# Kernel optimization log

Measured on AMD Instinct MI355X. Metric: run time of the kernel, lower is better.

## Reference

```python
import jax, jax.numpy as jnp
import numpy as np

NUM_EXPERTS = 8
HIDDEN = 1024
TOKENS = 8192


def setup_inputs() -> dict:
    key = jax.random.key(0)
    k1, k2, k3, k4 = jax.random.split(key, 4)
    inp = jax.random.normal(k1, (TOKENS, HIDDEN), dtype=jnp.float32)
    gate = jax.random.normal(k2, (TOKENS, NUM_EXPERTS), dtype=jnp.float32)
    # expert parameters: one dense layer per expert (H -> H)
    W = jax.random.normal(k3, (NUM_EXPERTS, HIDDEN, HIDDEN), dtype=jnp.float32) / np.sqrt(HIDDEN)
    b = jax.random.normal(k4, (NUM_EXPERTS, HIDDEN), dtype=jnp.float32) * 0.01
    return {"input": inp, "gate": gate, "W": W, "b": b}


def reference(input, gate, W, b):
    # Routing: softmax over router logits, top-1 expert per token.
    probs = jax.nn.softmax(gate, axis=-1)            # [T, E]
    expert_idx = jnp.argmax(probs, axis=-1)          # [T]
    top_p = jnp.take_along_axis(probs, expert_idx[:, None], axis=-1)[:, 0]  # [T]

    # Dispatch + grouped GEMM (computed densely for all experts, then masked):
    # y[e, t, d] = input[t, :] @ W[e] + b[e]
    y = jnp.einsum("th,ehd->etd", input, W) + b[:, None, :]  # [E, T, H]

    # Combine: select the routed expert's output, scaled by its gate prob.
    dispatch = jax.nn.one_hot(expert_idx, NUM_EXPERTS, dtype=input.dtype) * top_p[:, None]  # [T, E]
    out = jnp.einsum("etd,te->td", y, dispatch)      # [T, H]
    return out
```

## Files before the change

### kernel.cpp

```cpp
#include <hip/hip_runtime.h>
#include <hip/hip_bf16.h>
#include <cstdint>
#include <cstddef>

#define TOK 8192
#define HID 1024
#define NE 8

typedef __bf16 bf16x4 __attribute__((ext_vector_type(4)));
typedef __bf16 bf16x8 __attribute__((ext_vector_type(8)));
typedef float floatx4 __attribute__((ext_vector_type(4)));

static __device__ __forceinline__ __bf16 f2bf(float x) {
    unsigned u = __builtin_bit_cast(unsigned, x);
    u += 0x7fffu + ((u >> 16) & 1u);
    unsigned short hs = (unsigned short)(u >> 16);
    return __builtin_bit_cast(__bf16, hs);
}

__global__ void prep_kernel(const float* __restrict__ X, const float* __restrict__ gate,
                            const float* __restrict__ W,
                            __bf16* __restrict__ Xb, __bf16* __restrict__ Wt,
                            float* __restrict__ scale, int* __restrict__ counts,
                            int* __restrict__ list) {
    const int b = blockIdx.x;
    const int t = threadIdx.x;

    if (b < 4096) {
        size_t idx = (size_t)b * 256 + t;
        const float4 a0 = *(const float4*)(X + idx * 8);
        const float4 a1 = *(const float4*)(X + idx * 8 + 4);
        bf16x8 v;
        v[0] = f2bf(a0.x); v[1] = f2bf(a0.y); v[2] = f2bf(a0.z); v[3] = f2bf(a0.w);
        v[4] = f2bf(a1.x); v[5] = f2bf(a1.y); v[6] = f2bf(a1.z); v[7] = f2bf(a1.w);
        *(bf16x8*)(Xb + idx * 8) = v;

        if (b < 32) {
            __shared__ int hcnt[NE];
            __shared__ int hbase[NE];
            if (t < NE) hcnt[t] = 0;
            __syncthreads();
            int tok = b * 256 + t;
            float g[NE];
#pragma unroll
            for (int j = 0; j < NE; j++) g[j] = gate[tok * NE + j];
            float gm = g[0]; int best = 0;
#pragma unroll
            for (int j = 1; j < NE; j++) {
                if (g[j] > gm) { gm = g[j]; best = j; }
            }
            float s = 0.f;
#pragma unroll
            for (int j = 0; j < NE; j++) s += __expf(g[j] - gm);
            scale[tok] = 1.0f / s;
            int lpos = atomicAdd(&hcnt[best], 1);
            __syncthreads();
            if (t < NE) hbase[t] = atomicAdd(&counts[t], hcnt[t]);
            __syncthreads();
            list[best * TOK + hbase[best] + lpos] = tok;
        }
    } else {
        const int bb = b - 4096;
        const int e  = bb >> 6;
        const int kt = (bb >> 4) & 3;
        const int nt = bb & 15;
        const int k0 = kt * 256, n0 = nt * 64;
        const int ka = t >> 3;
        const int nb = t & 7;

        const float* src = W + ((size_t)e * HID + k0 + ka * 8) * HID + n0 + nb * 8;
        float rr[8][8];
#pragma unroll
        for (int i = 0; i < 8; i++) {
            float4 x = *(const float4*)(src + (size_t)i * HID);
            float4 y = *(const float4*)(src + (size_t)i * HID + 4);
            rr[i][0] = x.x; rr[i][1] = x.y; rr[i][2] = x.z; rr[i][3] = x.w;
            rr[i][4] = y.x; rr[i][5] = y.y; rr[i][6] = y.z; rr[i][7] = y.w;
        }
        __bf16* dst = Wt + ((size_t)e * HID + n0 + nb * 8) * HID + k0 + ka * 8;
#pragma unroll
        for (int j = 0; j < 8; j++) {
            bf16x8 v;
#pragma unroll
            for (int i = 0; i < 8; i++) v[i] = f2bf(rr[i][j]);
            *(bf16x8*)(dst + (size_t)j * HID) = v;
        }
    }
}

__launch_bounds__(256)
__global__ void moe_gemm_bf16(const __bf16* __restrict__ Xb, const __bf16* __restrict__ Wt,
                              const float* __restrict__ Bias, const float* __restrict__ scale,
                              const int* __restrict__ counts, const int* __restrict__ list,
                              float* __restrict__ out) {
    const int bid = blockIdx.x;
    const int e  = bid & 7;
    const int nt = (bid >> 3) & 15;
    const int mt = bid >> 7;

    const int cnt = counts[e];
    if (mt * 128 >= cnt) return;
    const int mvalid = min(128, cnt - mt * 128);
    const int n0 = nt * 64;

    __shared__ __bf16 As[128 * 64];
    __shared__ __bf16 Bs[64 * 64];
    __shared__ int   tok[128];
    __shared__ float scl[128];

    const int tid  = threadIdx.x;
    const int lane = tid & 63;
    const int wave = tid >> 6;

    if (tid < 128) {
        int g = mt * 128 + tid;
        int tk = (g < cnt) ? list[e * TOK + g] : 0;
        tok[tid] = tk;
        scl[tid] = (g < cnt) ? scale[tk] : 0.f;
    }
    __syncthreads();

    const int srow = lane >> 3;
    const int gchunk = ((lane & 7) ^ srow) * 8;
    const __bf16* aptr[4];
    const __bf16* bptr[2];
#pragma unroll
    for (int i = 0; i < 4; i++) {
        int r = wave * 32 + i * 8 + srow;
        aptr[i] = Xb + (size_t)tok[r] * HID + gchunk;
    }
#pragma unroll
    for (int i = 0; i < 2; i++) {
        int r = wave * 16 + i * 8 + srow;
        bptr[i] = Wt + ((size_t)e * HID + n0 + r) * HID + gchunk;
    }

    const int ln = lane & 15;
    const int q  = lane >> 4;
    const int wm = (wave >> 1) * 64;
    const int wn = (wave & 1) * 32;
    const int rsw = ln & 7;

    floatx4 acc[4][2];
#pragma unroll
    for (int mi = 0; mi < 4; mi++)
#pragma unroll
        for (int ni = 0; ni < 2; ni++) acc[mi][ni] = (floatx4){0.f, 0.f, 0.f, 0.f};

    for (int k0 = 0; k0 < HID; k0 += 64) {
#pragma unroll
        for (int i = 0; i < 4; i++)
            __builtin_amdgcn_global_load_lds(
                (const __attribute__((address_space(1))) void*)(aptr[i] + k0),
                (__attribute__((address_space(3))) void*)(&As[(wave * 32 + i * 8) * 64]),
                16, 0, 0);
#pragma unroll
        for (int i = 0; i < 2; i++)
            __builtin_amdgcn_global_load_lds(
                (const __attribute__((address_space(1))) void*)(bptr[i] + k0),
                (__attribute__((address_space(3))) void*)(&Bs[(wave * 16 + i * 8) * 64]),
                16, 0, 0);
        __syncthreads();

#pragma unroll
        for (int kk = 0; kk < 64; kk += 32) {
            const int cb = (kk >> 3) + q;
            const int pos = (cb ^ rsw) * 8;
            bf16x8 af[4], bfv[2];
#pragma unroll
            for (int mi = 0; mi < 4; mi++)
                af[mi] = *(const bf16x8*)(&As[(wm + mi * 16 + ln) * 64 + pos]);
#pragma unroll
            for (int ni = 0; ni < 2; ni++)
                bfv[ni] = *(const bf16x8*)(&Bs[(wn + ni * 16 + ln) * 64 + pos]);
#pragma unroll
            for (int mi = 0; mi < 4; mi++)
#pragma unroll
                for (int ni = 0; ni < 2; ni++)
                    acc[mi][ni] = __builtin_amdgcn_mfma_f32_16x16x32_bf16(
                        af[mi], bfv[ni], acc[mi][ni], 0, 0, 0);
        }
        __syncthreads();
    }

    float bn[2];
#pragma unroll
    for (int ni = 0; ni < 2; ni++) bn[ni] = Bias[e * HID + n0 + wn + ni * 16 + ln];

#pragma unroll
    for (int mi = 0; mi < 4; mi++) {
#pragma unroll
        for (int r = 0; r < 4; r++) {
            int row = wm + mi * 16 + q * 4 + r;
            if (row < mvalid) {
                int t = tok[row];
                float sc = scl[row];
                size_t ob = (size_t)t * HID + n0 + wn + ln;
#pragma unroll
                for (int ni = 0; ni < 2; ni++)
                    __builtin_nontemporal_store(sc * (acc[mi][ni][r] + bn[ni]),
                                                &out[ob + ni * 16]);
            }
        }
    }
}

__launch_bounds__(256)
__global__ void moe_gemm_fb(const float* __restrict__ X, const float* __restrict__ W,
                            const float* __restrict__ Bias, const float* __restrict__ scale,
                            const int* __restrict__ counts, const int* __restrict__ list,
                            float* __restrict__ out) {
    const int bid = blockIdx.x;
    const int e  = bid >> 9;
    const int nt = (bid >> 6) & 7;
    const int mt = bid & 63;
    const int cnt = counts[e];
    if (mt * 128 >= cnt) return;
    const int mvalid = min(128, cnt - mt * 128);
    const int n0 = nt * 128;

    __shared__ __bf16 As[128 * 64];
    __shared__ __bf16 Bs[128 * 64];
    __shared__ int   tok[128];
    __shared__ float scl[128];

    const int tid = threadIdx.x;
    if (tid < 128) {
        int g = mt * 128 + tid;
        int tk = (g < cnt) ? list[e * TOK + g] : 0;
        tok[tid] = tk;
        scl[tid] = (g < cnt) ? scale[tk] : 0.f;
    }
    __syncthreads();

    const int c4 = tid & 15;
    const float* rp[8];
    bool rv[8];
#pragma unroll
    for (int i = 0; i < 8; i++) {
        int m = (tid >> 4) + 16 * i;
        rv[i] = (m < mvalid);
        rp[i] = X + (size_t)tok[m] * HID;
    }
    const int n4 = tid & 31;
    const int kb = tid >> 5;
    const float* wbase = W + (size_t)e * HID * HID + (size_t)(kb * 8) * HID + n0 + n4 * 4;

    const int lane = tid & 63;
    const int ln = lane & 15;
    const int q  = lane >> 4;
    const int wave = tid >> 6;
    const int wm = (wave >> 1) * 64;
    const int wn = (wave & 1) * 64;

    floatx4 acc[4][4];
#pragma unroll
    for (int mi = 0; mi < 4; mi++)
#pragma unroll
        for (int ni = 0; ni < 4; ni++) acc[mi][ni] = (floatx4){0.f, 0.f, 0.f, 0.f};

    for (int k0 = 0; k0 < HID; k0 += 64) {
#pragma unroll
        for (int i = 0; i < 8; i++) {
            int m = (tid >> 4) + 16 * i;
            float4 v = make_float4(0.f, 0.f, 0.f, 0.f);
            if (rv[i]) v = *(const float4*)(rp[i] + k0 + c4 * 4);
            bf16x4 b4;
            b4[0] = f2bf(v.x); b4[1] = f2bf(v.y); b4[2] = f2bf(v.z); b4[3] = f2bf(v.w);
            int chunk = c4 >> 1;
            int addr = m * 64 + ((chunk ^ (m & 7)) * 8) + (c4 & 1) * 4;
            *(bf16x4*)(&As[addr]) = b4;
        }
        {
            const float* wp = wbase + (size_t)k0 * HID;
            float4 rr[8];
#pragma unroll
            for (int r = 0; r < 8; r++) rr[r] = *(const float4*)(wp + (size_t)r * HID);
#pragma unroll
            for (int j = 0; j < 4; j++) {
                int n = n4 * 4 + j;
                int c = kb ^ (n & 7);
                bf16x8 pk;
                pk[0] = f2bf(j == 0 ? rr[0].x : j == 1 ? rr[0].y : j == 2 ? rr[0].z : rr[0].w);
                pk[1] = f2bf(j == 0 ? rr[1].x : j == 1 ? rr[1].y : j == 2 ? rr[1].z : rr[1].w);
                pk[2] = f2bf(j == 0 ? rr[2].x : j == 1 ? rr[2].y : j == 2 ? rr[2].z : rr[2].w);
                pk[3] = f2bf(j == 0 ? rr[3].x : j == 1 ? rr[3].y : j == 2 ? rr[3].z : rr[3].w);
                pk[4] = f2bf(j == 0 ? rr[4].x : j == 1 ? rr[4].y : j == 2 ? rr[4].z : rr[4].w);
                pk[5] = f2bf(j == 0 ? rr[5].x : j == 1 ? rr[5].y : j == 2 ? rr[5].z : rr[5].w);
                pk[6] = f2bf(j == 0 ? rr[6].x : j == 1 ? rr[6].y : j == 2 ? rr[6].z : rr[6].w);
                pk[7] = f2bf(j == 0 ? rr[7].x : j == 1 ? rr[7].y : j == 2 ? rr[7].z : rr[7].w);
                *(bf16x8*)(&Bs[n * 64 + c * 8]) = pk;
            }
        }
        __syncthreads();
#pragma unroll
        for (int kk = 0; kk < 64; kk += 32) {
            const int cbase = (kk >> 3) + q;
            bf16x8 af[4], bfv[4];
#pragma unroll
            for (int mi = 0; mi < 4; mi++) {
                int row = wm + mi * 16 + ln;
                af[mi] = *(const bf16x8*)(&As[row * 64 + ((cbase ^ (row & 7)) * 8)]);
            }
#pragma unroll
            for (int ni = 0; ni < 4; ni++) {
                int n = wn + ni * 16 + ln;
                bfv[ni] = *(const bf16x8*)(&Bs[n * 64 + ((cbase ^ (n & 7)) * 8)]);
            }
#pragma unroll
            for (int mi = 0; mi < 4; mi++)
#pragma unroll
                for (int ni = 0; ni < 4; ni++)
                    acc[mi][ni] = __builtin_amdgcn_mfma_f32_16x16x32_bf16(
                        af[mi], bfv[ni], acc[mi][ni], 0, 0, 0);
        }
        __syncthreads();
    }

    float bn[4];
#pragma unroll
    for (int ni = 0; ni < 4; ni++) bn[ni] = Bias[e * HID + n0 + wn + ni * 16 + ln];
#pragma unroll
    for (int mi = 0; mi < 4; mi++) {
#pragma unroll
        for (int r = 0; r < 4; r++) {
            int row = wm + mi * 16 + q * 4 + r;
            if (row < mvalid) {
                int t = tok[row];
                float sc = scl[row];
                size_t ob = (size_t)t * HID + n0 + wn + ln;
#pragma unroll
                for (int ni = 0; ni < 4; ni++)
                    out[ob + ni * 16] = sc * (acc[mi][ni][r] + bn[ni]);
            }
        }
    }
}

__global__ void route_fb_kernel(const float* __restrict__ gate, float* __restrict__ scale,
                                int* __restrict__ counts, int* __restrict__ list) {
    int t = blockIdx.x * blockDim.x + threadIdx.x;
    if (t >= TOK) return;
    float g[NE];
#pragma unroll
    for (int j = 0; j < NE; j++) g[j] = gate[t * NE + j];
    float gm = g[0]; int best = 0;
#pragma unroll
    for (int j = 1; j < NE; j++) {
        if (g[j] > gm) { gm = g[j]; best = j; }
    }
    float s = 0.f;
#pragma unroll
    for (int j = 0; j < NE; j++) s += __expf(g[j] - gm);
    scale[t] = 1.0f / s;
    int pos = atomicAdd(&counts[best], 1);
    list[best * TOK + pos] = t;
}

extern "C" void kernel_launch(void* const* d_in, const int* in_sizes, int n_in,
                              void* d_out, int out_size, void* d_ws, size_t ws_size,
                              hipStream_t stream) {
    const float* X    = (const float*)d_in[0];
    const float* G    = (const float*)d_in[1];
    const float* W    = (const float*)d_in[2];
    const float* Bias = (const float*)d_in[3];
    float* out = (float*)d_out;

    float* scale = (float*)d_ws;
    int* counts  = (int*)((char*)d_ws + 32768);
    int* list    = (int*)((char*)d_ws + 36864);
    __bf16* Xb   = (__bf16*)((char*)d_ws + 299008);
    __bf16* Wt   = (__bf16*)((char*)d_ws + 299008 + 16777216);
    const size_t need = 299008 + 2 * 16777216ULL;

    hipMemsetAsync(counts, 0, NE * sizeof(int), stream);

    if (ws_size >= need) {
        prep_kernel<<<4608, 256, 0, stream>>>(X, G, W, Xb, Wt, scale, counts, list);
        moe_gemm_bf16<<<64 * 16 * 8, 256, 0, stream>>>(Xb, Wt, Bias, scale, counts, list, out);
    } else {
        route_fb_kernel<<<TOK / 256, 256, 0, stream>>>(G, scale, counts, list);
        moe_gemm_fb<<<NE * 64 * 8, 256, 0, stream>>>(X, W, Bias, scale, counts, list, out);
    }
}
```

Baseline: 145.9 us.

## Double-buffer LDS tiles in MoE GEMM to overlap global loads with MFMA

Splits the A and B shared-memory tiles into two buffers and prefetches the next K-tile with global_load_lds while MFMAs run on the current one. Each K step now has a single s_waitcnt plus barrier instead of two __syncthreads. This aims to hide global memory latency behind compute. It doubles LDS use per block to about 48KB, which can lower occupancy. Ordering relies on the single barrier also covering LDS reads of the buffer being refilled on the next iteration.

```diff
diff --git a/kernel.cpp b/kernel.cpp
--- a/kernel.cpp
+++ b/kernel.cpp
@@ -103,8 +103,8 @@
     const int mvalid = min(128, cnt - mt * 128);
     const int n0 = nt * 64;
 
-    __shared__ __bf16 As[128 * 64];
-    __shared__ __bf16 Bs[64 * 64];
+    __shared__ __bf16 As[2][128 * 64];
+    __shared__ __bf16 Bs[2][64 * 64];
     __shared__ int   tok[128];
     __shared__ float scl[128];
 
@@ -147,21 +147,22 @@
 #pragma unroll
         for (int ni = 0; ni < 2; ni++) acc[mi][ni] = (floatx4){0.f, 0.f, 0.f, 0.f};
 
-    for (int k0 = 0; k0 < HID; k0 += 64) {
+    auto stage = [&](int b, int k0) {
 #pragma unroll
         for (int i = 0; i < 4; i++)
             __builtin_amdgcn_global_load_lds(
                 (const __attribute__((address_space(1))) void*)(aptr[i] + k0),
-                (__attribute__((address_space(3))) void*)(&As[(wave * 32 + i * 8) * 64]),
+                (__attribute__((address_space(3))) void*)(&As[b][(wave * 32 + i * 8) * 64]),
                 16, 0, 0);
 #pragma unroll
         for (int i = 0; i < 2; i++)
             __builtin_amdgcn_global_load_lds(
                 (const __attribute__((address_space(1))) void*)(bptr[i] + k0),
-                (__attribute__((address_space(3))) void*)(&Bs[(wave * 16 + i * 8) * 64]),
+                (__attribute__((address_space(3))) void*)(&Bs[b][(wave * 16 + i * 8) * 64]),
                 16, 0, 0);
-        __syncthreads();
-
+    };
+
+    auto compute = [&](int b) {
 #pragma unroll
         for (int kk = 0; kk < 64; kk += 32) {
             const int cb = (kk >> 3) + q;
@@ -169,10 +170,10 @@
             bf16x8 af[4], bfv[2];
 #pragma unroll
             for (int mi = 0; mi < 4; mi++)
-                af[mi] = *(const bf16x8*)(&As[(wm + mi * 16 + ln) * 64 + pos]);
+                af[mi] = *(const bf16x8*)(&As[b][(wm + mi * 16 + ln) * 64 + pos]);
 #pragma unroll
             for (int ni = 0; ni < 2; ni++)
-                bfv[ni] = *(const bf16x8*)(&Bs[(wn + ni * 16 + ln) * 64 + pos]);
+                bfv[ni] = *(const bf16x8*)(&Bs[b][(wn + ni * 16 + ln) * 64 + pos]);
 #pragma unroll
             for (int mi = 0; mi < 4; mi++)
 #pragma unroll
@@ -180,8 +181,21 @@
                     acc[mi][ni] = __builtin_amdgcn_mfma_f32_16x16x32_bf16(
                         af[mi], bfv[ni], acc[mi][ni], 0, 0, 0);
         }
-        __syncthreads();
-    }
+    };
+
+    stage(0, 0);
+    asm volatile("s_waitcnt vmcnt(0)" ::: "memory");
+    __builtin_amdgcn_s_barrier();
+
+    int cur = 0;
+    for (int kt = 0; kt < 15; ++kt) {
+        stage(cur ^ 1, (kt + 1) * 64);
+        compute(cur);
+        asm volatile("s_waitcnt vmcnt(0)" ::: "memory");
+        __builtin_amdgcn_s_barrier();
+        cur ^= 1;
+    }
+    compute(cur);
 
     float bn[2];
 #pragma unroll
```

Measured after the change: 152.7 us. 4.7% more time.
